# Optimization experiments

Measured on AMD Instinct MI355X. Metric: run time of the kernel, lower is better.

Reference implementation:

```python
import jax, jax.numpy as jnp
import numpy as np

B, T, D = 32, 4096, 256   # batch, timesteps, input feature dim
H = 256                   # embed_dim (LSTM hidden size)
HORIZON = 24


def setup_inputs() -> dict:
    key = jax.random.key(0)
    ks = jax.random.split(key, 7)
    s_lstm = 1.0 / np.sqrt(D + H)
    s_fc = 1.0 / np.sqrt(H)
    return {
        "x": jax.random.normal(ks[0], (B, T, D), dtype=jnp.float32),
        # haiku hk.LSTM: single Linear on concat([x, h]) -> 4*H gates (i, g, f, o)
        "W_lstm": jax.random.uniform(ks[1], (D + H, 4 * H), jnp.float32, -s_lstm, s_lstm),
        "b_lstm": jnp.zeros((4 * H,), jnp.float32),
        "W_fc": jax.random.uniform(ks[2], (H, H), jnp.float32, -s_fc, s_fc),
        "b_fc": jnp.zeros((H,), jnp.float32),
        "W_out": jax.random.uniform(ks[3], (H, HORIZON), jnp.float32, -s_fc, s_fc),
        "b_out": jnp.zeros((HORIZON,), jnp.float32),
    }


def reference(x, W_lstm, b_lstm, W_fc, b_fc, W_out, b_out):
    b = x.shape[0]
    h0 = jnp.zeros((b, H), x.dtype)
    c0 = jnp.zeros((b, H), x.dtype)

    def step(carry, x_t):
        h, c = carry
        gates = jnp.concatenate([x_t, h], axis=-1) @ W_lstm + b_lstm  # [b, 4H]
        i, g, f, o = jnp.split(gates, 4, axis=-1)  # haiku gate order i, g, f, o
        c = jax.nn.sigmoid(f + 1.0) * c + jax.nn.sigmoid(i) * jnp.tanh(g)  # forget bias +1
        h = jax.nn.sigmoid(o) * jnp.tanh(c)
        return (h, c), None

    # scan over time: x -> [T, b, D]
    (h, _), _ = jax.lax.scan(step, (h0, c0), jnp.swapaxes(x, 0, 1))
    # reshape(x, (b, -1)) on [b, H] is a no-op
    out = h @ W_fc + b_fc
    out = out @ W_out + b_out
    return out  # [b, HORIZON]
```

## Files before the change

kernel.cpp:

```cpp
#include <hip/hip_runtime.h>
#include <hip/hip_fp16.h>


#define T_STEPS 4096
#define BATCH 32

typedef short short8 __attribute__((ext_vector_type(8)));
typedef float f32x4 __attribute__((ext_vector_type(4)));
typedef _Float16 half2_t __attribute__((ext_vector_type(2)));

__device__ inline unsigned short f32_to_bf16(float f) {
  unsigned int u = __builtin_bit_cast(unsigned int, f);
  u = u + 0x7fffu + ((u >> 16) & 1u);
  return (unsigned short)(u >> 16);
}

__device__ inline int dot4i8(unsigned int a, unsigned int b, int acc) {
#if __has_builtin(__builtin_amdgcn_sdot4)
  return __builtin_amdgcn_sdot4((int)a, (int)b, acc, false);
#else
  int r = acc;
#pragma unroll
  for (int k = 0; k < 4; ++k) {
    int av = (int)(signed char)((a >> (8 * k)) & 0xff);
    int bv = (int)(signed char)((b >> (8 * k)) & 0xff);
    r += av * bv;
  }
  return r;
#endif
}

__global__ void k_prep_x(const float4* __restrict__ x, unsigned short* __restrict__ xbf, int n4) {
  int i = blockIdx.x * blockDim.x + threadIdx.x;
  if (i >= n4) return;
  float4 v = x[i];
  ushort4 o;
  o.x = f32_to_bf16(v.x); o.y = f32_to_bf16(v.y);
  o.z = f32_to_bf16(v.z); o.w = f32_to_bf16(v.w);
  ((ushort4*)xbf)[i] = o;
}

__global__ void k_prep_wx(const float* __restrict__ W, unsigned short* __restrict__ WxT) {
  int i = blockIdx.x * blockDim.x + threadIdx.x;
  if (i >= 256 * 1024) return;
  int n = i >> 8, k = i & 255;
  WxT[i] = f32_to_bf16(W[k * 1024 + n]);
}

__global__ void k_prep_w8(const float* __restrict__ W, unsigned int* __restrict__ Wq8,
                          float* __restrict__ qs) {
  int c = blockIdx.x * blockDim.x + threadIdx.x;
  if (c >= 1024) return;
  float m = 0.0f;
  for (int k = 0; k < 256; ++k) m = fmaxf(m, fabsf(W[(256 + k) * 1024 + c]));
  if (m < 1e-20f) m = 1e-20f;
  float inv = 127.0f / m;
  int t, slot;
  if (c < 256)      { t = 2 * c;           slot = 0; }
  else if (c < 512) { t = 2 * (c - 256);   slot = 1; }
  else if (c < 768) { t = 2 * (c - 512) + 1; slot = 0; }
  else              { t = 2 * (c - 768) + 1; slot = 1; }
  for (int p4 = 0; p4 < 64; ++p4) {
    unsigned int d = 0;
    for (int b2 = 0; b2 < 4; ++b2) {
      float w = W[(256 + 4 * p4 + b2) * 1024 + c];
      int wi = (int)rintf(w * inv);
      wi = wi > 127 ? 127 : (wi < -127 ? -127 : wi);
      d |= ((unsigned int)(wi & 0xff)) << (8 * b2);
    }
    Wq8[p4 * 1024 + t * 2 + slot] = d;
  }
  qs[t * 2 + slot] = m / (127.0f * 127.0f);
}

__global__ __launch_bounds__(256) void k_xproj(const unsigned short* __restrict__ A,
                                               const unsigned short* __restrict__ BT,
                                               const float* __restrict__ bias,
                                               __half* __restrict__ G) {
  int bm = blockIdx.x * 64;
  int bn = blockIdx.y * 64;
  int lane = threadIdx.x & 63, wave = threadIdx.x >> 6;
  int wm = (wave & 1) * 32, wn = (wave >> 1) * 32;
  int q = lane >> 4, l16 = lane & 15;

  f32x4 acc[2][2] = {};
  const unsigned short* Ab = A + (size_t)(bm + wm + l16) * 256 + q * 8;
  const unsigned short* Bb = BT + (size_t)(bn + wn + l16) * 256 + q * 8;

#pragma unroll
  for (int kk = 0; kk < 8; ++kk) {
    short8 a0 = *(const short8*)(Ab + kk * 32);
    short8 a1 = *(const short8*)(Ab + 16 * 256 + kk * 32);
    short8 b0 = *(const short8*)(Bb + kk * 32);
    short8 b1 = *(const short8*)(Bb + 16 * 256 + kk * 32);
    acc[0][0] = __builtin_amdgcn_mfma_f32_16x16x32_bf16(a0, b0, acc[0][0], 0, 0, 0);
    acc[0][1] = __builtin_amdgcn_mfma_f32_16x16x32_bf16(a0, b1, acc[0][1], 0, 0, 0);
    acc[1][0] = __builtin_amdgcn_mfma_f32_16x16x32_bf16(a1, b0, acc[1][0], 0, 0, 0);
    acc[1][1] = __builtin_amdgcn_mfma_f32_16x16x32_bf16(a1, b1, acc[1][1], 0, 0, 0);
  }

#pragma unroll
  for (int nt = 0; nt < 2; ++nt) {
    int col = bn + wn + nt * 16 + l16;
    float bv = bias[col] + ((col >= 512 && col < 768) ? 1.0f : 0.0f);
    int gate = col >> 8, jj = col & 255;
#pragma unroll
    for (int mt = 0; mt < 2; ++mt) {
#pragma unroll
      for (int r = 0; r < 4; ++r) {
        int row = bm + wm + mt * 16 + q * 4 + r;
        G[(size_t)row * 1024 + jj * 4 + gate] = __float2half_rn(acc[mt][nt][r] + bv);
      }
    }
  }
}

__global__ __launch_bounds__(512, 2) void k_scan(const uint2* __restrict__ Wq8,
                                                 const float2* __restrict__ qs,
                                                 const __half* __restrict__ G,
                                                 float* __restrict__ hfin) {
  __shared__ __align__(16) unsigned int h8[2][64];

  int tid = threadIdx.x;
  int b = blockIdx.x;
  int j = tid >> 1;
  int odd = tid & 1;

  unsigned int wA[64], wB[64];
#pragma unroll
  for (int p4 = 0; p4 < 64; ++p4) {
    uint2 w = Wq8[p4 * 512 + tid];
    wA[p4] = w.x; wB[p4] = w.y;
  }
  float2 sc = qs[tid];

  if (tid < 64) { h8[0][tid] = 0u; }
  float cst = 0.0f;

  const unsigned short* gp = (const unsigned short*)G + (size_t)b * T_STEPS * 1024 + j * 4 + odd * 2;
  unsigned int gx_next = *(const unsigned int*)gp;
  __syncthreads();

  for (int step = 0; step < T_STEPS; ++step) {
    unsigned int gx_cur = gx_next;
    if (step + 1 < T_STEPS)
      gx_next = *(const unsigned int*)(gp + (size_t)(step + 1) * 1024);

    const uint4* hq = (const uint4*)h8[step & 1];

    int accA0 = 0, accB0 = 0, accA1 = 0, accB1 = 0;
#pragma unroll
    for (int ch = 0; ch < 16; ++ch) {
      uint4 hh = hq[ch];
      accA0 = dot4i8(wA[ch * 4 + 0], hh.x, accA0); accB0 = dot4i8(wB[ch * 4 + 0], hh.x, accB0);
      accA1 = dot4i8(wA[ch * 4 + 1], hh.y, accA1); accB1 = dot4i8(wB[ch * 4 + 1], hh.y, accB1);
      accA0 = dot4i8(wA[ch * 4 + 2], hh.z, accA0); accB0 = dot4i8(wB[ch * 4 + 2], hh.z, accB0);
      accA1 = dot4i8(wA[ch * 4 + 3], hh.w, accA1); accB1 = dot4i8(wB[ch * 4 + 3], hh.w, accB1);
    }

    half2_t gxh = __builtin_bit_cast(half2_t, gx_cur);
    float Av = (float)(accA0 + accA1) * sc.x + (float)gxh.x;
    float Bv = (float)(accB0 + accB1) * sc.y + (float)gxh.y;

    float sA = 1.0f / (1.0f + __expf(-Av));
    float eB = __expf(2.0f * Bv);
    float tB = 1.0f - 2.0f / (eB + 1.0f);
    float a = sA * tB;
    float a_x = __shfl_xor(a, 1, 64);
    if (odd) {
      float so = 1.0f / (1.0f + __expf(-Bv));
      cst = sA * cst + a_x;
      float ec = __expf(2.0f * cst);
      float tc = 1.0f - 2.0f / (ec + 1.0f);
      float h = so * tc;
      int hi = (int)rintf(h * 127.0f);
      ((char*)h8[(step + 1) & 1])[j] = (char)hi;
      if (step == T_STEPS - 1) hfin[b * 256 + j] = h;
    }

    asm volatile("s_waitcnt lgkmcnt(0)\n\ts_barrier" ::: "memory");
  }
}

__global__ void k_head(const float* __restrict__ hfin, const float* __restrict__ Wfc,
                       const float* __restrict__ bfc, const float* __restrict__ Wout,
                       const float* __restrict__ bout, float* __restrict__ out) {
  __shared__ float hs[256];
  __shared__ float fcs[256];
  int b = blockIdx.x, j = threadIdx.x;
  hs[j] = hfin[b * 256 + j];
  __syncthreads();
  float acc = bfc[j];
#pragma unroll 8
  for (int k = 0; k < 256; ++k) acc += hs[k] * Wfc[k * 256 + j];
  fcs[j] = acc;
  __syncthreads();
  if (j < 24) {
    float a2 = bout[j];
#pragma unroll 8
    for (int k = 0; k < 256; ++k) a2 += fcs[k] * Wout[k * 24 + j];
    out[b * 24 + j] = a2;
  }
}

extern "C" void kernel_launch(void* const* d_in, const int* in_sizes, int n_in,
                              void* d_out, int out_size, void* d_ws, size_t ws_size,
                              hipStream_t stream) {
  const float* x    = (const float*)d_in[0];
  const float* Wl   = (const float*)d_in[1];
  const float* bl   = (const float*)d_in[2];
  const float* Wfc  = (const float*)d_in[3];
  const float* bfc  = (const float*)d_in[4];
  const float* Wout = (const float*)d_in[5];
  const float* bout = (const float*)d_in[6];
  float* out = (float*)d_out;

  char* ws = (char*)d_ws;
  unsigned short* xbf = (unsigned short*)ws;
  unsigned short* WxT = (unsigned short*)(ws + 67108864);
  unsigned int*   Wq8 = (unsigned int*)(ws + 67633152);
  float*          qsb = (float*)(ws + 67895296);
  __half*         G   = (__half*)(ws + 68157440);
  float*          hfin= (float*)(ws + 336592896);

  k_prep_x<<<32768, 256, 0, stream>>>((const float4*)x, xbf, 8388608);
  k_prep_wx<<<1024, 256, 0, stream>>>(Wl, WxT);
  k_prep_w8<<<4, 256, 0, stream>>>(Wl, Wq8, qsb);
  dim3 gx(2048, 16, 1);
  k_xproj<<<gx, 256, 0, stream>>>(xbf, WxT, bl, G);
  k_scan<<<32, 512, 0, stream>>>((const uint2*)Wq8, (const float2*)qsb, G, hfin);
  k_head<<<32, 256, 0, stream>>>(hfin, Wfc, bfc, Wout, bout, out);
}
```

Baseline: 4.717 ms.

## Split recurrent dot product over K halves per thread pair, all four gates per thread

The scan kernel's work split changes. Each thread pair previously owned two gates over the full K=256. Now each thread computes all four gates over half of K, and the halves are combined with xor shuffles, so both threads of a pair can evaluate the cell update redundantly without exchanging gate activations. The int8 weight prep kernel is also rewritten to run one wave per column with a shuffle max reduction instead of a serial loop over 4 small blocks. The cost is four shuffles per step instead of one, plus duplicated transcendental work in every thread.

```diff
diff --git a/kernel.cpp b/kernel.cpp
--- a/kernel.cpp
+++ b/kernel.cpp
@@ -47,30 +47,37 @@
   WxT[i] = f32_to_bf16(W[k * 1024 + n]);
 }
 
-__global__ void k_prep_w8(const float* __restrict__ W, unsigned int* __restrict__ Wq8,
-                          float* __restrict__ qs) {
-  int c = blockIdx.x * blockDim.x + threadIdx.x;
-  if (c >= 1024) return;
-  float m = 0.0f;
-  for (int k = 0; k < 256; ++k) m = fmaxf(m, fabsf(W[(256 + k) * 1024 + c]));
-  if (m < 1e-20f) m = 1e-20f;
-  float inv = 127.0f / m;
-  int t, slot;
-  if (c < 256)      { t = 2 * c;           slot = 0; }
-  else if (c < 512) { t = 2 * (c - 256);   slot = 1; }
-  else if (c < 768) { t = 2 * (c - 512) + 1; slot = 0; }
-  else              { t = 2 * (c - 768) + 1; slot = 1; }
-  for (int p4 = 0; p4 < 64; ++p4) {
-    unsigned int d = 0;
-    for (int b2 = 0; b2 < 4; ++b2) {
-      float w = W[(256 + 4 * p4 + b2) * 1024 + c];
-      int wi = (int)rintf(w * inv);
-      wi = wi > 127 ? 127 : (wi < -127 ? -127 : wi);
-      d |= ((unsigned int)(wi & 0xff)) << (8 * b2);
-    }
-    Wq8[p4 * 1024 + t * 2 + slot] = d;
-  }
-  qs[t * 2 + slot] = m / (127.0f * 127.0f);
+__global__ __launch_bounds__(512) void k_prep_w8(const float* __restrict__ W,
+                                                 unsigned int* __restrict__ Wq4,
+                                                 float* __restrict__ qs4) {
+  int c = blockIdx.x * 8 + (threadIdx.x >> 6);
+  int l = threadIdx.x & 63;
+  int gate = c >> 8, jj = c & 255;
+
+  float w0 = W[(256 + 4 * l + 0) * 1024 + c];
+  float w1 = W[(256 + 4 * l + 1) * 1024 + c];
+  float w2 = W[(256 + 4 * l + 2) * 1024 + c];
+  float w3 = W[(256 + 4 * l + 3) * 1024 + c];
+  float mm = fmaxf(fmaxf(fabsf(w0), fabsf(w1)), fmaxf(fabsf(w2), fabsf(w3)));
+#pragma unroll
+  for (int s = 32; s; s >>= 1) mm = fmaxf(mm, __shfl_xor(mm, s, 64));
+  if (mm < 1e-20f) mm = 1e-20f;
+  float inv = 127.0f / mm;
+
+  int q0 = (int)rintf(w0 * inv); q0 = q0 > 127 ? 127 : (q0 < -127 ? -127 : q0);
+  int q1 = (int)rintf(w1 * inv); q1 = q1 > 127 ? 127 : (q1 < -127 ? -127 : q1);
+  int q2 = (int)rintf(w2 * inv); q2 = q2 > 127 ? 127 : (q2 < -127 ? -127 : q2);
+  int q3 = (int)rintf(w3 * inv); q3 = q3 > 127 ? 127 : (q3 < -127 ? -127 : q3);
+  unsigned int d = (unsigned int)(q0 & 0xff) | ((unsigned int)(q1 & 0xff) << 8) |
+                   ((unsigned int)(q2 & 0xff) << 16) | ((unsigned int)(q3 & 0xff) << 24);
+
+  int kh = l >> 5, p4 = l & 31;
+  Wq4[((p4 * 512) + (jj * 2 + kh)) * 4 + gate] = d;
+  if (l == 0) {
+    float s = mm / (127.0f * 127.0f);
+    qs4[(jj * 2 + 0) * 4 + gate] = s;
+    qs4[(jj * 2 + 1) * 4 + gate] = s;
+  }
 }
 
 __global__ __launch_bounds__(256) void k_xproj(const unsigned short* __restrict__ A,
@@ -115,8 +122,8 @@
   }
 }
 
-__global__ __launch_bounds__(512, 2) void k_scan(const uint2* __restrict__ Wq8,
-                                                 const float2* __restrict__ qs,
+__global__ __launch_bounds__(512, 2) void k_scan(const unsigned int* __restrict__ Wq4,
+                                                 const float* __restrict__ qs4,
                                                  const __half* __restrict__ G,
                                                  float* __restrict__ hfin) {
   __shared__ __align__(16) unsigned int h8[2][64];
@@ -124,55 +131,70 @@
   int tid = threadIdx.x;
   int b = blockIdx.x;
   int j = tid >> 1;
-  int odd = tid & 1;
-
-  unsigned int wA[64], wB[64];
-#pragma unroll
-  for (int p4 = 0; p4 < 64; ++p4) {
-    uint2 w = Wq8[p4 * 512 + tid];
-    wA[p4] = w.x; wB[p4] = w.y;
-  }
-  float2 sc = qs[tid];
-
-  if (tid < 64) { h8[0][tid] = 0u; }
+  int kh = tid & 1;
+
+  unsigned int wI[32], wG[32], wF[32], wO[32];
+  {
+    const uint4* wqp = (const uint4*)Wq4;
+#pragma unroll
+    for (int p4 = 0; p4 < 32; ++p4) {
+      uint4 w = wqp[p4 * 512 + tid];
+      wI[p4] = w.x; wG[p4] = w.y; wF[p4] = w.z; wO[p4] = w.w;
+    }
+  }
+  float4 sc = *(const float4*)(qs4 + tid * 4);
+
+  if (tid < 64) h8[0][tid] = 0u;
   float cst = 0.0f;
 
-  const unsigned short* gp = (const unsigned short*)G + (size_t)b * T_STEPS * 1024 + j * 4 + odd * 2;
-  unsigned int gx_next = *(const unsigned int*)gp;
+  const unsigned short* gp = (const unsigned short*)G + (size_t)b * T_STEPS * 1024 + j * 4;
+  uint2 gx_next = *(const uint2*)gp;
   __syncthreads();
 
   for (int step = 0; step < T_STEPS; ++step) {
-    unsigned int gx_cur = gx_next;
+    uint2 gx_cur = gx_next;
     if (step + 1 < T_STEPS)
-      gx_next = *(const unsigned int*)(gp + (size_t)(step + 1) * 1024);
+      gx_next = *(const uint2*)(gp + (size_t)(step + 1) * 1024);
 
     const uint4* hq = (const uint4*)h8[step & 1];
 
-    int accA0 = 0, accB0 = 0, accA1 = 0, accB1 = 0;
-#pragma unroll
-    for (int ch = 0; ch < 16; ++ch) {
-      uint4 hh = hq[ch];
-      accA0 = dot4i8(wA[ch * 4 + 0], hh.x, accA0); accB0 = dot4i8(wB[ch * 4 + 0], hh.x, accB0);
-      accA1 = dot4i8(wA[ch * 4 + 1], hh.y, accA1); accB1 = dot4i8(wB[ch * 4 + 1], hh.y, accB1);
-      accA0 = dot4i8(wA[ch * 4 + 2], hh.z, accA0); accB0 = dot4i8(wB[ch * 4 + 2], hh.z, accB0);
-      accA1 = dot4i8(wA[ch * 4 + 3], hh.w, accA1); accB1 = dot4i8(wB[ch * 4 + 3], hh.w, accB1);
-    }
-
-    half2_t gxh = __builtin_bit_cast(half2_t, gx_cur);
-    float Av = (float)(accA0 + accA1) * sc.x + (float)gxh.x;
-    float Bv = (float)(accB0 + accB1) * sc.y + (float)gxh.y;
-
-    float sA = 1.0f / (1.0f + __expf(-Av));
-    float eB = __expf(2.0f * Bv);
-    float tB = 1.0f - 2.0f / (eB + 1.0f);
-    float a = sA * tB;
-    float a_x = __shfl_xor(a, 1, 64);
-    if (odd) {
-      float so = 1.0f / (1.0f + __expf(-Bv));
-      cst = sA * cst + a_x;
-      float ec = __expf(2.0f * cst);
-      float tc = 1.0f - 2.0f / (ec + 1.0f);
-      float h = so * tc;
+    int aI = 0, aG = 0, aF = 0, aO = 0;
+#pragma unroll
+    for (int ch = 0; ch < 8; ++ch) {
+      uint4 hh = hq[kh * 8 + ch];
+      aI = dot4i8(wI[ch * 4 + 0], hh.x, aI); aG = dot4i8(wG[ch * 4 + 0], hh.x, aG);
+      aF = dot4i8(wF[ch * 4 + 0], hh.x, aF); aO = dot4i8(wO[ch * 4 + 0], hh.x, aO);
+      aI = dot4i8(wI[ch * 4 + 1], hh.y, aI); aG = dot4i8(wG[ch * 4 + 1], hh.y, aG);
+      aF = dot4i8(wF[ch * 4 + 1], hh.y, aF); aO = dot4i8(wO[ch * 4 + 1], hh.y, aO);
+      aI = dot4i8(wI[ch * 4 + 2], hh.z, aI); aG = dot4i8(wG[ch * 4 + 2], hh.z, aG);
+      aF = dot4i8(wF[ch * 4 + 2], hh.z, aF); aO = dot4i8(wO[ch * 4 + 2], hh.z, aO);
+      aI = dot4i8(wI[ch * 4 + 3], hh.w, aI); aG = dot4i8(wG[ch * 4 + 3], hh.w, aG);
+      aF = dot4i8(wF[ch * 4 + 3], hh.w, aF); aO = dot4i8(wO[ch * 4 + 3], hh.w, aO);
+    }
+
+    aI += __shfl_xor(aI, 1, 64);
+    aG += __shfl_xor(aG, 1, 64);
+    aF += __shfl_xor(aF, 1, 64);
+    aO += __shfl_xor(aO, 1, 64);
+
+    half2_t g01 = __builtin_bit_cast(half2_t, gx_cur.x);
+    half2_t g23 = __builtin_bit_cast(half2_t, gx_cur.y);
+    float gi = (float)aI * sc.x + (float)g01.x;
+    float gg = (float)aG * sc.y + (float)g01.y;
+    float gf = (float)aF * sc.z + (float)g23.x;
+    float go = (float)aO * sc.w + (float)g23.y;
+
+    float si = 1.0f / (1.0f + __expf(-gi));
+    float sf = 1.0f / (1.0f + __expf(-gf));
+    float so = 1.0f / (1.0f + __expf(-go));
+    float eg = __expf(2.0f * gg);
+    float tg = 1.0f - 2.0f / (eg + 1.0f);
+    cst = sf * cst + si * tg;
+    float ec = __expf(2.0f * cst);
+    float tc = 1.0f - 2.0f / (ec + 1.0f);
+    float h = so * tc;
+
+    if (!kh) {
       int hi = (int)rintf(h * 127.0f);
       ((char*)h8[(step + 1) & 1])[j] = (char)hi;
       if (step == T_STEPS - 1) hfin[b * 256 + j] = h;
@@ -218,16 +240,16 @@
   char* ws = (char*)d_ws;
   unsigned short* xbf = (unsigned short*)ws;
   unsigned short* WxT = (unsigned short*)(ws + 67108864);
-  unsigned int*   Wq8 = (unsigned int*)(ws + 67633152);
+  unsigned int*   Wq4 = (unsigned int*)(ws + 67633152);
   float*          qsb = (float*)(ws + 67895296);
   __half*         G   = (__half*)(ws + 68157440);
   float*          hfin= (float*)(ws + 336592896);
 
   k_prep_x<<<32768, 256, 0, stream>>>((const float4*)x, xbf, 8388608);
   k_prep_wx<<<1024, 256, 0, stream>>>(Wl, WxT);
-  k_prep_w8<<<4, 256, 0, stream>>>(Wl, Wq8, qsb);
+  k_prep_w8<<<128, 512, 0, stream>>>(Wl, Wq4, qsb);
   dim3 gx(2048, 16, 1);
   k_xproj<<<gx, 256, 0, stream>>>(xbf, WxT, bl, G);
-  k_scan<<<32, 512, 0, stream>>>((const uint2*)Wq8, (const float2*)qsb, G, hfin);
+  k_scan<<<32, 512, 0, stream>>>(Wq4, qsb, G, hfin);
   k_head<<<32, 256, 0, stream>>>(hfin, Wfc, bfc, Wout, bout, out);
 }
```

Measured after the change: 4.848 ms. 2.8% more time.

## Enlarge xproj MFMA tile to 64x256 and parallelize int8 weight quantization

Applied to the files above, without the earlier changes.

The x-projection GEMM now gives each block a 64x256 output tile, with each wave computing a 64x64 sub-tile of 16 MFMA accumulators instead of 32x32. Each loaded A/B fragment is therefore reused more often and less global-load traffic is spent per MFMA. The cost is higher register pressure, which may lower occupancy. Separately, the recurrent-weight quantization kernel changes from 1024 serial threads to one wave per column, using a shuffle max-reduction, to cut its long serial latency.

```diff
diff --git a/kernel.cpp b/kernel.cpp
--- a/kernel.cpp
+++ b/kernel.cpp
@@ -47,30 +47,36 @@
   WxT[i] = f32_to_bf16(W[k * 1024 + n]);
 }
 
-__global__ void k_prep_w8(const float* __restrict__ W, unsigned int* __restrict__ Wq8,
-                          float* __restrict__ qs) {
-  int c = blockIdx.x * blockDim.x + threadIdx.x;
-  if (c >= 1024) return;
-  float m = 0.0f;
-  for (int k = 0; k < 256; ++k) m = fmaxf(m, fabsf(W[(256 + k) * 1024 + c]));
-  if (m < 1e-20f) m = 1e-20f;
-  float inv = 127.0f / m;
+__global__ __launch_bounds__(512) void k_prep_w8(const float* __restrict__ W,
+                                                 unsigned int* __restrict__ Wq8,
+                                                 float* __restrict__ qs) {
+  int c = blockIdx.x * 8 + (threadIdx.x >> 6);
+  int l = threadIdx.x & 63;
+
+  float w0 = W[(256 + 4 * l + 0) * 1024 + c];
+  float w1 = W[(256 + 4 * l + 1) * 1024 + c];
+  float w2 = W[(256 + 4 * l + 2) * 1024 + c];
+  float w3 = W[(256 + 4 * l + 3) * 1024 + c];
+  float mm = fmaxf(fmaxf(fabsf(w0), fabsf(w1)), fmaxf(fabsf(w2), fabsf(w3)));
+#pragma unroll
+  for (int s = 32; s; s >>= 1) mm = fmaxf(mm, __shfl_xor(mm, s, 64));
+  if (mm < 1e-20f) mm = 1e-20f;
+  float inv = 127.0f / mm;
+
+  int q0 = (int)rintf(w0 * inv); q0 = q0 > 127 ? 127 : (q0 < -127 ? -127 : q0);
+  int q1 = (int)rintf(w1 * inv); q1 = q1 > 127 ? 127 : (q1 < -127 ? -127 : q1);
+  int q2 = (int)rintf(w2 * inv); q2 = q2 > 127 ? 127 : (q2 < -127 ? -127 : q2);
+  int q3 = (int)rintf(w3 * inv); q3 = q3 > 127 ? 127 : (q3 < -127 ? -127 : q3);
+  unsigned int d = (unsigned int)(q0 & 0xff) | ((unsigned int)(q1 & 0xff) << 8) |
+                   ((unsigned int)(q2 & 0xff) << 16) | ((unsigned int)(q3 & 0xff) << 24);
+
   int t, slot;
-  if (c < 256)      { t = 2 * c;           slot = 0; }
-  else if (c < 512) { t = 2 * (c - 256);   slot = 1; }
+  if (c < 256)      { t = 2 * c;             slot = 0; }
+  else if (c < 512) { t = 2 * (c - 256);     slot = 1; }
   else if (c < 768) { t = 2 * (c - 512) + 1; slot = 0; }
   else              { t = 2 * (c - 768) + 1; slot = 1; }
-  for (int p4 = 0; p4 < 64; ++p4) {
-    unsigned int d = 0;
-    for (int b2 = 0; b2 < 4; ++b2) {
-      float w = W[(256 + 4 * p4 + b2) * 1024 + c];
-      int wi = (int)rintf(w * inv);
-      wi = wi > 127 ? 127 : (wi < -127 ? -127 : wi);
-      d |= ((unsigned int)(wi & 0xff)) << (8 * b2);
-    }
-    Wq8[p4 * 1024 + t * 2 + slot] = d;
-  }
-  qs[t * 2 + slot] = m / (127.0f * 127.0f);
+  Wq8[l * 1024 + t * 2 + slot] = d;
+  if (l == 0) qs[t * 2 + slot] = mm / (127.0f * 127.0f);
 }
 
 __global__ __launch_bounds__(256) void k_xproj(const unsigned short* __restrict__ A,
@@ -78,37 +84,39 @@
                                                const float* __restrict__ bias,
                                                __half* __restrict__ G) {
   int bm = blockIdx.x * 64;
-  int bn = blockIdx.y * 64;
+  int bn = blockIdx.y * 256;
   int lane = threadIdx.x & 63, wave = threadIdx.x >> 6;
-  int wm = (wave & 1) * 32, wn = (wave >> 1) * 32;
+  int wn = wave * 64;
   int q = lane >> 4, l16 = lane & 15;
 
-  f32x4 acc[2][2] = {};
-  const unsigned short* Ab = A + (size_t)(bm + wm + l16) * 256 + q * 8;
+  f32x4 acc[4][4] = {};
+  const unsigned short* Ab = A + (size_t)(bm + l16) * 256 + q * 8;
   const unsigned short* Bb = BT + (size_t)(bn + wn + l16) * 256 + q * 8;
 
 #pragma unroll
   for (int kk = 0; kk < 8; ++kk) {
-    short8 a0 = *(const short8*)(Ab + kk * 32);
-    short8 a1 = *(const short8*)(Ab + 16 * 256 + kk * 32);
-    short8 b0 = *(const short8*)(Bb + kk * 32);
-    short8 b1 = *(const short8*)(Bb + 16 * 256 + kk * 32);
-    acc[0][0] = __builtin_amdgcn_mfma_f32_16x16x32_bf16(a0, b0, acc[0][0], 0, 0, 0);
-    acc[0][1] = __builtin_amdgcn_mfma_f32_16x16x32_bf16(a0, b1, acc[0][1], 0, 0, 0);
-    acc[1][0] = __builtin_amdgcn_mfma_f32_16x16x32_bf16(a1, b0, acc[1][0], 0, 0, 0);
-    acc[1][1] = __builtin_amdgcn_mfma_f32_16x16x32_bf16(a1, b1, acc[1][1], 0, 0, 0);
-  }
-
-#pragma unroll
-  for (int nt = 0; nt < 2; ++nt) {
+    short8 a[4], bf[4];
+#pragma unroll
+    for (int mt = 0; mt < 4; ++mt) a[mt] = *(const short8*)(Ab + mt * 16 * 256 + kk * 32);
+#pragma unroll
+    for (int nt = 0; nt < 4; ++nt) bf[nt] = *(const short8*)(Bb + nt * 16 * 256 + kk * 32);
+#pragma unroll
+    for (int mt = 0; mt < 4; ++mt)
+#pragma unroll
+      for (int nt = 0; nt < 4; ++nt)
+        acc[mt][nt] = __builtin_amdgcn_mfma_f32_16x16x32_bf16(a[mt], bf[nt], acc[mt][nt], 0, 0, 0);
+  }
+
+#pragma unroll
+  for (int nt = 0; nt < 4; ++nt) {
     int col = bn + wn + nt * 16 + l16;
     float bv = bias[col] + ((col >= 512 && col < 768) ? 1.0f : 0.0f);
     int gate = col >> 8, jj = col & 255;
 #pragma unroll
-    for (int mt = 0; mt < 2; ++mt) {
+    for (int mt = 0; mt < 4; ++mt) {
 #pragma unroll
       for (int r = 0; r < 4; ++r) {
-        int row = bm + wm + mt * 16 + q * 4 + r;
+        int row = bm + mt * 16 + q * 4 + r;
         G[(size_t)row * 1024 + jj * 4 + gate] = __float2half_rn(acc[mt][nt][r] + bv);
       }
     }
@@ -225,8 +233,8 @@
 
   k_prep_x<<<32768, 256, 0, stream>>>((const float4*)x, xbf, 8388608);
   k_prep_wx<<<1024, 256, 0, stream>>>(Wl, WxT);
-  k_prep_w8<<<4, 256, 0, stream>>>(Wl, Wq8, qsb);
-  dim3 gx(2048, 16, 1);
+  k_prep_w8<<<128, 512, 0, stream>>>(Wl, Wq8, qsb);
+  dim3 gx(2048, 4, 1);
   k_xproj<<<gx, 256, 0, stream>>>(xbf, WxT, bl, G);
   k_scan<<<32, 512, 0, stream>>>((const uint2*)Wq8, (const float2*)qsb, G, hfin);
   k_head<<<32, 256, 0, stream>>>(hfin, Wfc, bfc, Wout, bout, out);
```

Result: faster. 4.552 ms (-3.5%).
